# Performance work log

Measured on AMD Instinct MI355X. Metric: run time of the kernel, lower is better.

The kernel has to match this reference:

```python
import jax, jax.numpy as jnp
import numpy as np
from jax import lax

NUM_SAMPLE_POINTS = 1024
BIG = jnp.float32(1e10)  # stands in for +inf, fp16-safe


def setup_inputs() -> dict:
    key = jax.random.key(0)
    input = jax.random.normal(key, (8, 65536, 3), dtype=jnp.float32)
    return {"input": input}


def _fps_indices(points, num_samples):
    # points: [B, N, 3] -> indices [B, num_samples] int32
    B, N, _ = points.shape

    def step(carry, _):
        min_dist, farthest = carry  # [B, N], [B]
        cur = jnp.take_along_axis(points, farthest[:, None, None], axis=1)  # [B,1,3]
        d = jnp.sum((points - cur) ** 2, axis=-1)  # [B, N] squared distances
        min_dist = jnp.minimum(min_dist, d)
        nxt = jnp.argmax(min_dist, axis=-1).astype(jnp.int32)  # [B]
        return (min_dist, nxt), farthest

    init = (jnp.full((B, N), BIG, dtype=points.dtype), jnp.zeros((B,), jnp.int32))
    _, idx = lax.scan(step, init, None, length=num_samples)  # idx: [M, B]
    return idx.T  # [B, M]


def reference(input):
    # Faithful FPS: iteratively pick the point farthest from the selected set,
    # starting from index 0 (standard PointNet++ convention).
    idx = _fps_indices(input, NUM_SAMPLE_POINTS)  # [B, M] int32
    sampled = jnp.take_along_axis(input, idx[:, :, None], axis=1)  # [B, M, 3]
    return idx, sampled
```

## Files before the change

kernel.cpp:

```cpp
#include <hip/hip_runtime.h>


#define NB    8
#define NPTS  65536
#define NSAMP 1024
#define WPB   8
#define TPB   1024
#define PPT   8
#define RECQ  16

typedef unsigned long long ull;

__device__ __forceinline__ void ld3_sc0(const ull* p, ull& a, ull& b, ull& c) {
  asm volatile(
      "global_load_dwordx2 %0, %3, off sc0\n\t"
      "global_load_dwordx2 %1, %3, off offset:8 sc0\n\t"
      "global_load_dwordx2 %2, %3, off offset:16 sc0\n\t"
      "s_waitcnt vmcnt(0)"
      : "=&v"(a), "=&v"(b), "=&v"(c) : "v"(p) : "memory");
}

__device__ __forceinline__ void st3_sc0(ull* p, ull a, ull b, ull c) {
  asm volatile(
      "global_store_dwordx2 %3, %0, off sc0\n\t"
      "global_store_dwordx2 %3, %1, off offset:8 sc0\n\t"
      "global_store_dwordx2 %3, %2, off offset:16 sc0"
      :: "v"(a), "v"(b), "v"(c), "v"(p) : "memory");
}

__global__ __launch_bounds__(TPB, 4)
void fps_kernel(const float* __restrict__ pts, float* __restrict__ out,
                ull* __restrict__ ws) {
  const int wg   = blockIdx.x;
  const int b    = wg >> 3;
  const int w    = wg & 7;
  const int tid  = threadIdx.x;
  const int lane = tid & 63;
  const int wave = tid >> 6;

  const float* p = pts + (size_t)b * NPTS * 3;

  float px[PPT], py[PPT], pz[PPT], md[PPT];
#pragma unroll
  for (int i = 0; i < PPT; ++i) {
    const int n = w * (TPB * PPT) + i * TPB + tid;
    px[i] = p[3 * n + 0];
    py[i] = p[3 * n + 1];
    pz[i] = p[3 * n + 2];
    md[i] = 1e10f;
  }

  float cx = p[0], cy = p[1], cz = p[2];

  ull* baseL = ws + (size_t)b * (2 * WPB * RECQ);
  ull* baseI = ws + (size_t)NB * (2 * WPB * RECQ) + (size_t)b * (2 * WPB * RECQ);

  float* out_idx = out + (size_t)b * NSAMP;
  float* out_smp = out + (size_t)NB * NSAMP + (size_t)b * NSAMP * 3;

  if (w == 0 && tid == 0) {
    out_idx[0] = 0.0f;
    out_smp[0] = cx; out_smp[1] = cy; out_smp[2] = cz;
  }

  __shared__ unsigned red[16][5];
  __shared__ float bc[3];

  bool useIF = false;

  for (int t = 0; t < NSAMP - 1; ++t) {
    float bv = -1.0f; int bi = 0; float bx = 0.f, by = 0.f, bz = 0.f;
#pragma unroll
    for (int i = 0; i < PPT; ++i) {
      const float dx = __fsub_rn(px[i], cx);
      const float dy = __fsub_rn(py[i], cy);
      const float dz = __fsub_rn(pz[i], cz);
      const float d  = __fadd_rn(__fadd_rn(__fmul_rn(dx, dx), __fmul_rn(dy, dy)),
                                 __fmul_rn(dz, dz));
      const float m = fminf(md[i], d);
      md[i] = m;
      if (m > bv) {
        bv = m; bi = i;
        bx = px[i]; by = py[i]; bz = pz[i];
      }
    }

    float maxd = bv;
#pragma unroll
    for (int s = 1; s < 64; s <<= 1) {
      const float o = __shfl_xor(maxd, s, 64);
      maxd = fmaxf(maxd, o);
    }
    const bool tied = (bv == maxd);
    const ull bal0 = __ballot(tied);
    int wlane;
    if (__popcll(bal0) == 1) {
      wlane = __ffsll(bal0) - 1;
    } else {
      ull sel = 0;
#pragma unroll
      for (int ii = 0; ii < PPT; ++ii) {
        const ull bb = __ballot(tied && (bi == ii));
        const bool take = (sel == 0) && (bb != 0);
        sel = take ? bb : sel;
      }
      wlane = __ffsll(sel) - 1;
    }
    if (lane == wlane) {
      red[wave][0] = __float_as_uint(bv);
      red[wave][1] = (unsigned)(w * (TPB * PPT) + bi * TPB + tid);
      red[wave][2] = __float_as_uint(bx);
      red[wave][3] = __float_as_uint(by);
      red[wave][4] = __float_as_uint(bz);
    }
    __syncthreads();

    const ull tag = (ull)(unsigned)(t + 1);
    const int par = t & 1;

    if (wave == 0) {
      const int e = lane & 15;
      const unsigned d2 = red[e][0];
      const unsigned nn = red[e][1];
      unsigned m2 = d2;
#pragma unroll
      for (int s = 1; s < 16; s <<= 1) {
        const unsigned o = __shfl_xor(m2, s, 64);
        m2 = o > m2 ? o : m2;
      }
      const ull bb = __ballot(d2 == m2) & 0xFFFFull;
      int ewin;
      if (__popcll(bb) == 1) {
        ewin = __ffsll(bb) - 1;
      } else {
        const unsigned v = (d2 == m2) ? (65535u - nn) : 0u;
        unsigned mv = v;
#pragma unroll
        for (int s = 1; s < 16; s <<= 1) {
          const unsigned o = __shfl_xor(mv, s, 64);
          mv = o > mv ? o : mv;
        }
        const ull b2 = __ballot((d2 == m2) && (v == mv)) & 0xFFFFull;
        ewin = __ffsll(b2) - 1;
      }
      if (lane == ewin) {
        const ull k2 = ((ull)d2 << 16) | (ull)(65535u - nn);
        const unsigned xb = red[e][2], yb = red[e][3], zb = red[e][4];
        const ull w0 = (k2 << 16) | tag;
        const ull w1 = ((ull)xb << 32) | ((ull)(yb >> 16) << 16) | tag;
        const ull w2 = ((ull)(yb & 0xFFFFu) << 48) | ((ull)zb << 16) | tag;
        st3_sc0(baseL + (size_t)(par * WPB + w) * RECQ, w0, w1, w2);
      }

      const size_t roff = (size_t)(par * WPB + (lane & 7)) * RECQ;
      const ull* recL = baseL + roff;
      const ull* recI = baseI + roff;
      const bool mine = (lane < WPB);
      bool done = !mine;
      ull r0 = 0, r1 = 0, r2 = 0;
      int spins = 0;
      for (;;) {
        if (!done) {
          if (!useIF) {
            ld3_sc0(recL, r0, r1, r2);
          } else {
            r0 = __hip_atomic_load(recI + 0, __ATOMIC_RELAXED, __HIP_MEMORY_SCOPE_AGENT);
            r1 = __hip_atomic_load(recI + 1, __ATOMIC_RELAXED, __HIP_MEMORY_SCOPE_AGENT);
            r2 = __hip_atomic_load(recI + 2, __ATOMIC_RELAXED, __HIP_MEMORY_SCOPE_AGENT);
          }
          done = ((r0 & 0xFFFFull) == tag) & ((r1 & 0xFFFFull) == tag) &
                 ((r2 & 0xFFFFull) == tag);
          if (!done && !useIF && ++spins > 256) useIF = true;
        }
        if (__all(done)) break;
        if (useIF) __builtin_amdgcn_s_sleep(1);
      }

      const unsigned d3  = (unsigned)(r0 >> 32);
      const unsigned lnv = (unsigned)((r0 >> 16) & 0xFFFFull);
      unsigned m3 = d3;
#pragma unroll
      for (int s = 1; s < 8; s <<= 1) {
        const unsigned o = __shfl_xor(m3, s, 64);
        m3 = o > m3 ? o : m3;
      }
      const ull b3 = __ballot(d3 == m3) & 0xFFull;
      int src;
      if (__popcll(b3) == 1) {
        src = __ffsll(b3) - 1;
      } else {
        const unsigned v = (d3 == m3) ? lnv : 0u;
        unsigned mv = v;
#pragma unroll
        for (int s = 1; s < 8; s <<= 1) {
          const unsigned o = __shfl_xor(mv, s, 64);
          mv = o > mv ? o : mv;
        }
        const ull b4 = __ballot((d3 == m3) && (v == mv)) & 0xFFull;
        src = __ffsll(b4) - 1;
      }
      const float xx = __uint_as_float((unsigned)(r1 >> 32));
      const float yy = __uint_as_float(((unsigned)((r1 >> 16) & 0xFFFFull) << 16) |
                                       (unsigned)(r2 >> 48));
      const float zz = __uint_as_float((unsigned)((r2 >> 16) & 0xFFFFFFFFull));
      const int n2   = 65535 - (int)__shfl(lnv, src, 64);
      const float wx = __shfl(xx, src, 64);
      const float wy = __shfl(yy, src, 64);
      const float wz = __shfl(zz, src, 64);
      if (lane == 0) {
        bc[0] = wx; bc[1] = wy; bc[2] = wz;
        if (w == 0) {
          out_idx[t + 1] = (float)n2;
          out_smp[(t + 1) * 3 + 0] = wx;
          out_smp[(t + 1) * 3 + 1] = wy;
          out_smp[(t + 1) * 3 + 2] = wz;
        }
      }
    } else if (wave == 1) {
      const int e = lane & 15;
      const unsigned d2 = red[e][0];
      const unsigned nn = red[e][1];
      unsigned m2 = d2;
#pragma unroll
      for (int s = 1; s < 16; s <<= 1) {
        const unsigned o = __shfl_xor(m2, s, 64);
        m2 = o > m2 ? o : m2;
      }
      const ull bb = __ballot(d2 == m2) & 0xFFFFull;
      int ewin;
      if (__popcll(bb) == 1) {
        ewin = __ffsll(bb) - 1;
      } else {
        const unsigned v = (d2 == m2) ? (65535u - nn) : 0u;
        unsigned mv = v;
#pragma unroll
        for (int s = 1; s < 16; s <<= 1) {
          const unsigned o = __shfl_xor(mv, s, 64);
          mv = o > mv ? o : mv;
        }
        const ull b2 = __ballot((d2 == m2) && (v == mv)) & 0xFFFFull;
        ewin = __ffsll(b2) - 1;
      }
      if (lane == ewin) {
        const ull k2 = ((ull)d2 << 16) | (ull)(65535u - nn);
        const unsigned xb = red[e][2], yb = red[e][3], zb = red[e][4];
        const ull w0 = (k2 << 16) | tag;
        const ull w1 = ((ull)xb << 32) | ((ull)(yb >> 16) << 16) | tag;
        const ull w2 = ((ull)(yb & 0xFFFFu) << 48) | ((ull)zb << 16) | tag;
        ull* recI = baseI + (size_t)(par * WPB + w) * RECQ;
        __hip_atomic_store(recI + 0, w0, __ATOMIC_RELAXED, __HIP_MEMORY_SCOPE_AGENT);
        __hip_atomic_store(recI + 1, w1, __ATOMIC_RELAXED, __HIP_MEMORY_SCOPE_AGENT);
        __hip_atomic_store(recI + 2, w2, __ATOMIC_RELAXED, __HIP_MEMORY_SCOPE_AGENT);
      }
    }
    __syncthreads();
    cx = bc[0]; cy = bc[1]; cz = bc[2];
  }
}

extern "C" void kernel_launch(void* const* d_in, const int* in_sizes, int n_in,
                              void* d_out, int out_size, void* d_ws, size_t ws_size,
                              hipStream_t stream) {
  (void)in_sizes; (void)n_in; (void)out_size; (void)ws_size;
  const float* pts = (const float*)d_in[0];
  float* out = (float*)d_out;
  ull* ws = (ull*)d_ws;
  fps_kernel<<<dim3(NB * WPB), dim3(TPB), 0, stream>>>(pts, out, ws);
}
```

Baseline: 2.513 ms.

## Replace workgroup barriers with LDS counter/flag handoff and DPP max reductions

Removes both __syncthreads per iteration. An LDS atomic counter lets the last-arriving wave perform the stage-2 reduction and publish the record, and an LDS flag broadcasts the chosen centroid to the waiting waves. Wave-level max reductions switch from shuffles to DPP row ops plus readlane. The change cuts barrier latency on the serial critical path. In exchange, non-zero waves spin on LDS, and correctness depends on the memory ordering of the acquire/release atomics within the workgroup.

```diff
diff --git a/kernel.cpp b/kernel.cpp
--- a/kernel.cpp
+++ b/kernel.cpp
@@ -11,6 +11,35 @@
 
 typedef unsigned long long ull;
 
+#define DPP(x, ctrl) \
+  ((unsigned)__builtin_amdgcn_update_dpp((int)(x), (int)(x), (ctrl), 0xf, 0xf, false))
+
+__device__ __forceinline__ unsigned umax_wave64(unsigned x) {
+  unsigned t;
+  t = DPP(x, 0x111); x = t > x ? t : x;
+  t = DPP(x, 0x112); x = t > x ? t : x;
+  t = DPP(x, 0x114); x = t > x ? t : x;
+  t = DPP(x, 0x118); x = t > x ? t : x;
+  t = DPP(x, 0x142); x = t > x ? t : x;
+  t = DPP(x, 0x143); x = t > x ? t : x;
+  return (unsigned)__builtin_amdgcn_readlane((int)x, 63);
+}
+__device__ __forceinline__ unsigned umax_row16(unsigned x) {
+  unsigned t;
+  t = DPP(x, 0x111); x = t > x ? t : x;
+  t = DPP(x, 0x112); x = t > x ? t : x;
+  t = DPP(x, 0x114); x = t > x ? t : x;
+  t = DPP(x, 0x118); x = t > x ? t : x;
+  return (unsigned)__builtin_amdgcn_readlane((int)x, 15);
+}
+__device__ __forceinline__ unsigned umax_low8(unsigned x) {
+  unsigned t;
+  t = DPP(x, 0x111); x = t > x ? t : x;
+  t = DPP(x, 0x112); x = t > x ? t : x;
+  t = DPP(x, 0x114); x = t > x ? t : x;
+  return (unsigned)__builtin_amdgcn_readlane((int)x, 7);
+}
+
 __device__ __forceinline__ void ld3_sc0(const ull* p, ull& a, ull& b, ull& c) {
   asm volatile(
       "global_load_dwordx2 %0, %3, off sc0\n\t"
@@ -19,13 +48,35 @@
       "s_waitcnt vmcnt(0)"
       : "=&v"(a), "=&v"(b), "=&v"(c) : "v"(p) : "memory");
 }
-
 __device__ __forceinline__ void st3_sc0(ull* p, ull a, ull b, ull c) {
   asm volatile(
       "global_store_dwordx2 %3, %0, off sc0\n\t"
       "global_store_dwordx2 %3, %1, off offset:8 sc0\n\t"
       "global_store_dwordx2 %3, %2, off offset:16 sc0"
       :: "v"(a), "v"(b), "v"(c), "v"(p) : "memory");
+}
+
+__device__ __forceinline__ void stage2_pack(const unsigned red[16][5], int lane,
+                                            ull tag, ull& w0, ull& w1, ull& w2,
+                                            int& ewin) {
+  const int e = lane & 15;
+  const unsigned d2 = red[e][0];
+  const unsigned nn = red[e][1];
+  const unsigned mx = umax_row16(d2);
+  const ull bb = __ballot(d2 == mx) & 0xFFFFull;
+  if (__popcll(bb) == 1) {
+    ewin = __ffsll(bb) - 1;
+  } else {
+    const unsigned v = (d2 == mx) ? (65535u - nn) : 0u;
+    const unsigned mv = umax_row16(v);
+    const ull b2 = __ballot((d2 == mx) && (v == mv)) & 0xFFFFull;
+    ewin = __ffsll(b2) - 1;
+  }
+  const ull k2 = ((ull)d2 << 16) | (ull)(65535u - nn);
+  const unsigned xb = red[e][2], yb = red[e][3], zb = red[e][4];
+  w0 = (k2 << 16) | tag;
+  w1 = ((ull)xb << 32) | ((ull)(yb >> 16) << 16) | tag;
+  w2 = ((ull)(yb & 0xFFFFu) << 48) | ((ull)zb << 16) | tag;
 }
 
 __global__ __launch_bounds__(TPB, 4)
@@ -65,6 +116,11 @@
 
   __shared__ unsigned red[16][5];
   __shared__ float bc[3];
+  __shared__ int cnt;
+  __shared__ int flag;
+
+  if (tid == 0) { cnt = 0; flag = 0; }
+  __syncthreads();
 
   bool useIF = false;
 
@@ -85,13 +141,9 @@
       }
     }
 
-    float maxd = bv;
-#pragma unroll
-    for (int s = 1; s < 64; s <<= 1) {
-      const float o = __shfl_xor(maxd, s, 64);
-      maxd = fmaxf(maxd, o);
-    }
-    const bool tied = (bv == maxd);
+    const unsigned dbits = __float_as_uint(bv);
+    const unsigned mw = umax_wave64(dbits);
+    const bool tied = (dbits == mw);
     const ull bal0 = __ballot(tied);
     int wlane;
     if (__popcll(bal0) == 1) {
@@ -107,51 +159,29 @@
       wlane = __ffsll(sel) - 1;
     }
     if (lane == wlane) {
-      red[wave][0] = __float_as_uint(bv);
+      red[wave][0] = dbits;
       red[wave][1] = (unsigned)(w * (TPB * PPT) + bi * TPB + tid);
       red[wave][2] = __float_as_uint(bx);
       red[wave][3] = __float_as_uint(by);
       red[wave][4] = __float_as_uint(bz);
     }
-    __syncthreads();
 
     const ull tag = (ull)(unsigned)(t + 1);
     const int par = t & 1;
 
+    int ret = 0;
+    if (lane == 0)
+      ret = __hip_atomic_fetch_add(&cnt, 1, __ATOMIC_ACQ_REL,
+                                   __HIP_MEMORY_SCOPE_WORKGROUP);
+    const int isLast = __shfl((int)(ret == 16 * t + 15), 0, 64);
+    if (isLast) {
+      ull w0, w1, w2; int ewin;
+      stage2_pack(red, lane, tag, w0, w1, w2, ewin);
+      if (lane == ewin)
+        st3_sc0(baseL + (size_t)(par * WPB + w) * RECQ, w0, w1, w2);
+    }
+
     if (wave == 0) {
-      const int e = lane & 15;
-      const unsigned d2 = red[e][0];
-      const unsigned nn = red[e][1];
-      unsigned m2 = d2;
-#pragma unroll
-      for (int s = 1; s < 16; s <<= 1) {
-        const unsigned o = __shfl_xor(m2, s, 64);
-        m2 = o > m2 ? o : m2;
-      }
-      const ull bb = __ballot(d2 == m2) & 0xFFFFull;
-      int ewin;
-      if (__popcll(bb) == 1) {
-        ewin = __ffsll(bb) - 1;
-      } else {
-        const unsigned v = (d2 == m2) ? (65535u - nn) : 0u;
-        unsigned mv = v;
-#pragma unroll
-        for (int s = 1; s < 16; s <<= 1) {
-          const unsigned o = __shfl_xor(mv, s, 64);
-          mv = o > mv ? o : mv;
-        }
-        const ull b2 = __ballot((d2 == m2) && (v == mv)) & 0xFFFFull;
-        ewin = __ffsll(b2) - 1;
-      }
-      if (lane == ewin) {
-        const ull k2 = ((ull)d2 << 16) | (ull)(65535u - nn);
-        const unsigned xb = red[e][2], yb = red[e][3], zb = red[e][4];
-        const ull w0 = (k2 << 16) | tag;
-        const ull w1 = ((ull)xb << 32) | ((ull)(yb >> 16) << 16) | tag;
-        const ull w2 = ((ull)(yb & 0xFFFFu) << 48) | ((ull)zb << 16) | tag;
-        st3_sc0(baseL + (size_t)(par * WPB + w) * RECQ, w0, w1, w2);
-      }
-
       const size_t roff = (size_t)(par * WPB + (lane & 7)) * RECQ;
       const ull* recL = baseL + roff;
       const ull* recI = baseI + roff;
@@ -178,24 +208,14 @@
 
       const unsigned d3  = (unsigned)(r0 >> 32);
       const unsigned lnv = (unsigned)((r0 >> 16) & 0xFFFFull);
-      unsigned m3 = d3;
-#pragma unroll
-      for (int s = 1; s < 8; s <<= 1) {
-        const unsigned o = __shfl_xor(m3, s, 64);
-        m3 = o > m3 ? o : m3;
-      }
+      const unsigned m3 = umax_low8(d3);
       const ull b3 = __ballot(d3 == m3) & 0xFFull;
       int src;
       if (__popcll(b3) == 1) {
         src = __ffsll(b3) - 1;
       } else {
         const unsigned v = (d3 == m3) ? lnv : 0u;
-        unsigned mv = v;
-#pragma unroll
-        for (int s = 1; s < 8; s <<= 1) {
-          const unsigned o = __shfl_xor(mv, s, 64);
-          mv = o > mv ? o : mv;
-        }
+        const unsigned mv = umax_low8(v);
         const ull b4 = __ballot((d3 == m3) && (v == mv)) & 0xFFull;
         src = __ffsll(b4) - 1;
       }
@@ -203,12 +223,14 @@
       const float yy = __uint_as_float(((unsigned)((r1 >> 16) & 0xFFFFull) << 16) |
                                        (unsigned)(r2 >> 48));
       const float zz = __uint_as_float((unsigned)((r2 >> 16) & 0xFFFFFFFFull));
-      const int n2   = 65535 - (int)__shfl(lnv, src, 64);
+      const int n2   = 65535 - (int)__shfl((int)lnv, src, 64);
       const float wx = __shfl(xx, src, 64);
       const float wy = __shfl(yy, src, 64);
       const float wz = __shfl(zz, src, 64);
       if (lane == 0) {
         bc[0] = wx; bc[1] = wy; bc[2] = wz;
+        __hip_atomic_store(&flag, t + 1, __ATOMIC_RELEASE,
+                           __HIP_MEMORY_SCOPE_WORKGROUP);
         if (w == 0) {
           out_idx[t + 1] = (float)n2;
           out_smp[(t + 1) * 3 + 0] = wx;
@@ -216,45 +238,24 @@
           out_smp[(t + 1) * 3 + 2] = wz;
         }
       }
-    } else if (wave == 1) {
-      const int e = lane & 15;
-      const unsigned d2 = red[e][0];
-      const unsigned nn = red[e][1];
-      unsigned m2 = d2;
-#pragma unroll
-      for (int s = 1; s < 16; s <<= 1) {
-        const unsigned o = __shfl_xor(m2, s, 64);
-        m2 = o > m2 ? o : m2;
-      }
-      const ull bb = __ballot(d2 == m2) & 0xFFFFull;
-      int ewin;
-      if (__popcll(bb) == 1) {
-        ewin = __ffsll(bb) - 1;
-      } else {
-        const unsigned v = (d2 == m2) ? (65535u - nn) : 0u;
-        unsigned mv = v;
-#pragma unroll
-        for (int s = 1; s < 16; s <<= 1) {
-          const unsigned o = __shfl_xor(mv, s, 64);
-          mv = o > mv ? o : mv;
+      cx = wx; cy = wy; cz = wz;
+    } else {
+      if (wave == 15) {
+        while (__hip_atomic_load(&cnt, __ATOMIC_ACQUIRE,
+                                 __HIP_MEMORY_SCOPE_WORKGROUP) < 16 * (t + 1)) {}
+        ull w0, w1, w2; int ewin;
+        stage2_pack(red, lane, tag, w0, w1, w2, ewin);
+        if (lane == ewin) {
+          ull* recI = baseI + (size_t)(par * WPB + w) * RECQ;
+          __hip_atomic_store(recI + 0, w0, __ATOMIC_RELAXED, __HIP_MEMORY_SCOPE_AGENT);
+          __hip_atomic_store(recI + 1, w1, __ATOMIC_RELAXED, __HIP_MEMORY_SCOPE_AGENT);
+          __hip_atomic_store(recI + 2, w2, __ATOMIC_RELAXED, __HIP_MEMORY_SCOPE_AGENT);
         }
-        const ull b2 = __ballot((d2 == m2) && (v == mv)) & 0xFFFFull;
-        ewin = __ffsll(b2) - 1;
-      }
-      if (lane == ewin) {
-        const ull k2 = ((ull)d2 << 16) | (ull)(65535u - nn);
-        const unsigned xb = red[e][2], yb = red[e][3], zb = red[e][4];
-        const ull w0 = (k2 << 16) | tag;
-        const ull w1 = ((ull)xb << 32) | ((ull)(yb >> 16) << 16) | tag;
-        const ull w2 = ((ull)(yb & 0xFFFFu) << 48) | ((ull)zb << 16) | tag;
-        ull* recI = baseI + (size_t)(par * WPB + w) * RECQ;
-        __hip_atomic_store(recI + 0, w0, __ATOMIC_RELAXED, __HIP_MEMORY_SCOPE_AGENT);
-        __hip_atomic_store(recI + 1, w1, __ATOMIC_RELAXED, __HIP_MEMORY_SCOPE_AGENT);
-        __hip_atomic_store(recI + 2, w2, __ATOMIC_RELAXED, __HIP_MEMORY_SCOPE_AGENT);
-      }
-    }
-    __syncthreads();
-    cx = bc[0]; cy = bc[1]; cz = bc[2];
+      }
+      while (__hip_atomic_load(&flag, __ATOMIC_ACQUIRE,
+                               __HIP_MEMORY_SCOPE_WORKGROUP) < t + 1) {}
+      cx = bc[0]; cy = bc[1]; cz = bc[2];
+    }
   }
 }
 
```

After: 2.630 ms. 4.7% more time.
